# Kernel optimization log

Hardware: AMD Instinct MI355X
Metric: run time of the kernel (lower is better)

Reference implementation:

```python
import jax, jax.numpy as jnp
import numpy as np

N = 100000      # nodes
E = 1600000     # edges
F_IN = 128
HID = 64
N_CLS = 40


def setup_inputs() -> dict:
    key = jax.random.key(0)
    ks = jax.random.split(key, 8)
    x = jax.random.normal(ks[0], (N, F_IN), dtype=jnp.float32)
    edge_index = jax.random.randint(ks[1], (2, E), 0, N, dtype=jnp.int64)
    # SAGEConv params: lin_l (applied to mean-aggregated neighbors, with bias),
    # lin_r (applied to root/self features, no bias). Glorot-ish init scaling.
    W1_l = jax.random.normal(ks[2], (F_IN, HID), dtype=jnp.float32) / np.sqrt(F_IN)
    b1 = jnp.zeros((HID,), dtype=jnp.float32)
    W1_r = jax.random.normal(ks[3], (F_IN, HID), dtype=jnp.float32) / np.sqrt(F_IN)
    W2_l = jax.random.normal(ks[4], (HID, N_CLS), dtype=jnp.float32) / np.sqrt(HID)
    b2 = jnp.zeros((N_CLS,), dtype=jnp.float32)
    W2_r = jax.random.normal(ks[5], (HID, N_CLS), dtype=jnp.float32) / np.sqrt(HID)
    return {"x": x, "edge_index": edge_index,
            "W1_l": W1_l, "b1": b1, "W1_r": W1_r,
            "W2_l": W2_l, "b2": b2, "W2_r": W2_r}


def _sage_conv(x, src, dst, W_l, b_l, W_r):
    # mean aggregation of neighbor features: messages flow src -> dst
    msgs = x[src]                                              # [E, d]
    summed = jax.ops.segment_sum(msgs, dst, num_segments=N)    # [N, d]
    cnt = jax.ops.segment_sum(jnp.ones((src.shape[0],), x.dtype), dst,
                              num_segments=N)                  # [N]
    agg = summed / jnp.maximum(cnt, 1.0)[:, None]
    return agg @ W_l + b_l + x @ W_r


def reference(x, edge_index, W1_l, b1, W1_r, W2_l, b2, W2_r):
    src, dst = edge_index[0], edge_index[1]
    h = jax.nn.relu(_sage_conv(x, src, dst, W1_l, b1, W1_r))
    # dropout: identity in eval mode
    logits = _sage_conv(h, src, dst, W2_l, b2, W2_r)
    return jax.nn.log_softmax(logits, axis=1)
```

## Files before the change

### kernel.cpp

```cpp
#include <hip/hip_runtime.h>
#include <math.h>

#define N_NODES 100000
#define F_IN    128
#define HID     64
#define N_CLS   40
#define MT      (N_NODES / 16)

#define BSHIFT  9
#define BSZ     512
#define NB      ((N_NODES + BSZ - 1) / BSZ)
#define EPB     4096

typedef __attribute__((ext_vector_type(8))) short bf8_t;
typedef __attribute__((ext_vector_type(4))) float f4_t;
typedef __attribute__((ext_vector_type(2))) float f2v_t;

typedef unsigned short ushort_t;
typedef unsigned int uint_t;
typedef unsigned char uchar_t;

__device__ __forceinline__ ushort_t f2b(float f) {
    union { float f; uint_t u; } c; c.f = f;
    uint_t u = c.u + 0x7FFFu + ((c.u >> 16) & 1u);
    return (ushort_t)(u >> 16);
}
__device__ __forceinline__ float b2f(ushort_t h) {
    union { uint_t u; float f; } c; c.u = ((uint_t)h) << 16;
    return c.f;
}

#if defined(__has_builtin)
#if __has_builtin(__builtin_amdgcn_cvt_pk_f32_fp8) && __has_builtin(__builtin_amdgcn_cvt_pk_fp8_f32)
#define HAVE_FP8_HW 1
#endif
#endif

__device__ __forceinline__ uchar_t fp8_enc(float v) {
#ifdef HAVE_FP8_HW
    return (uchar_t)(__builtin_amdgcn_cvt_pk_fp8_f32(v, v, 0, false) & 0xff);
#else
    union { float f; uint_t u; } c; c.f = v;
    uint_t s = c.u >> 31;
    float av = fabsf(v);
    if (av > 448.f) av = 448.f;
    int e;
    float m = frexpf(av, &e);
    int ee = e + 6;
    uchar_t r;
    if (av == 0.f) r = 0;
    else if (ee <= 0) {
        int q = (int)(av * 512.f + 0.5f);
        if (q > 7) q = 7;
        r = (uchar_t)q;
    } else {
        int q = (int)(m * 16.f + 0.5f);
        if (q == 16) { q = 8; ee += 1; }
        if (ee > 15) { ee = 15; q = 15; }
        r = (uchar_t)((ee << 3) | (q & 7));
    }
    return r | (uchar_t)(s << 7);
#endif
}

__device__ __forceinline__ f2v_t fp8x2_dec_lo(uint_t w) {
#ifdef HAVE_FP8_HW
    return __builtin_amdgcn_cvt_pk_f32_fp8(w, false);
#else
    f2v_t r;
    for (int k = 0; k < 2; ++k) {
        uchar_t b = (w >> (8 * k)) & 0xff;
        uint_t s = (b >> 7) & 1, e = (b >> 3) & 15, m = b & 7;
        float f;
        if (e) { union { uint_t u; float ff; } c;
                 c.u = (s << 31) | ((e + 120) << 23) | (m << 20); f = c.ff; }
        else   { f = (float)m * 0.001953125f; if (s) f = -f; }
        r[k] = f;
    }
    return r;
#endif
}
__device__ __forceinline__ f2v_t fp8x2_dec_hi(uint_t w) {
#ifdef HAVE_FP8_HW
    return __builtin_amdgcn_cvt_pk_f32_fp8(w, true);
#else
    return fp8x2_dec_lo(w >> 16);
#endif
}

__global__ void block_hist_kernel(const int* __restrict__ ei, int E,
                                  int* __restrict__ blockHist) {
    __shared__ int cnt[NB];
    int t = threadIdx.x, blk = blockIdx.x;
    for (int i = t; i < NB; i += 256) cnt[i] = 0;
    __syncthreads();
    int e0 = blk * EPB;
#pragma unroll
    for (int i = 0; i < EPB / 256; ++i) {
        int e = e0 + i * 256 + t;
        if (e < E) atomicAdd(&cnt[ei[E + e] >> BSHIFT], 1);
    }
    __syncthreads();
    for (int i = t; i < NB; i += 256) blockHist[blk * NB + i] = cnt[i];
}

__global__ void col_scan_kernel(const int* __restrict__ blockHist, int nblk,
                                int* __restrict__ blockBase,
                                int* __restrict__ btot) {
    __shared__ int ss[256];
    __shared__ int carry;
    int bin = blockIdx.x, t = threadIdx.x;
    if (t == 0) carry = 0;
    __syncthreads();
    for (int c0 = 0; c0 < nblk; c0 += 256) {
        int b = c0 + t;
        int v = (b < nblk) ? blockHist[b * NB + bin] : 0;
        ss[t] = v;
        __syncthreads();
        for (int off = 1; off < 256; off <<= 1) {
            int u = (t >= off) ? ss[t - off] : 0;
            __syncthreads();
            ss[t] += u;
            __syncthreads();
        }
        if (b < nblk) blockBase[b * NB + bin] = carry + ss[t] - v;
        __syncthreads();
        if (t == 255) carry += ss[255];
        __syncthreads();
    }
    if (t == 0) btot[bin] = carry;
}

__global__ void scatter_pairs_kernel(const int* __restrict__ ei, int E,
                                     const int* __restrict__ blockBase,
                                     const int* __restrict__ btot,
                                     uint_t* __restrict__ pairs) {
    __shared__ int cur[NB];
    __shared__ int base[NB];
    __shared__ int ss[256];
    int t = threadIdx.x, blk = blockIdx.x;
    int v = (t < NB) ? btot[t] : 0;
    ss[t] = v;
    __syncthreads();
    for (int off = 1; off < 256; off <<= 1) {
        int u = (t >= off) ? ss[t - off] : 0;
        __syncthreads();
        ss[t] += u;
        __syncthreads();
    }
    if (t < NB) {
        cur[t] = 0;
        base[t] = (ss[t] - v) + blockBase[blk * NB + t];
    }
    __syncthreads();
    int e0 = blk * EPB;
#pragma unroll
    for (int i = 0; i < EPB / 256; ++i) {
        int e = e0 + i * 256 + t;
        if (e < E) {
            int src = ei[e];
            int dst = ei[E + e];
            int bin = dst >> BSHIFT;
            int r = atomicAdd(&cur[bin], 1);
            pairs[base[bin] + r] = ((uint_t)src << BSHIFT) | (uint_t)(dst & (BSZ - 1));
        }
    }
}

__global__ void bucket_sort_kernel(const uint_t* __restrict__ pairs,
                                   const int* __restrict__ btot,
                                   int* __restrict__ rowptr,
                                   int* __restrict__ csr) {
    __shared__ int hist[BSZ];
    __shared__ int lofs[BSZ];
    int bin = blockIdx.x, t = threadIdx.x;
    int pv = (t < NB) ? btot[t] : 0;
    lofs[t] = pv;
    __syncthreads();
    for (int off = 1; off < BSZ; off <<= 1) {
        int u = (t >= off) ? lofs[t - off] : 0;
        __syncthreads();
        lofs[t] += u;
        __syncthreads();
    }
    int base = (bin > 0) ? lofs[bin - 1] : 0;
    int cnt = btot[bin];
    __syncthreads();
    hist[t] = 0;
    __syncthreads();
    for (int i = t; i < cnt; i += BSZ)
        atomicAdd(&hist[pairs[base + i] & (BSZ - 1)], 1);
    __syncthreads();
    int v = hist[t];
    lofs[t] = v;
    __syncthreads();
    for (int off = 1; off < BSZ; off <<= 1) {
        int u = (t >= off) ? lofs[t - off] : 0;
        __syncthreads();
        lofs[t] += u;
        __syncthreads();
    }
    int excl = lofs[t] - v;
    int d_global = (bin << BSHIFT) + t;
    if (d_global < N_NODES) rowptr[d_global] = base + excl;
    if (bin == NB - 1 && t == 0) rowptr[N_NODES] = base + cnt;
    __syncthreads();
    lofs[t] = excl;
    hist[t] = 0;
    __syncthreads();
    for (int i = t; i < cnt; i += BSZ) {
        uint_t p = pairs[base + i];
        int lb = p & (BSZ - 1);
        int r = atomicAdd(&hist[lb], 1);
        csr[base + lofs[lb] + r] = (int)(p >> BSHIFT);
    }
}

__global__ void cvt_w_kernel(const float* __restrict__ W1l,
                             const float* __restrict__ W1r,
                             const float* __restrict__ W2l,
                             const float* __restrict__ W2r,
                             ushort_t* __restrict__ W1t,
                             ushort_t* __restrict__ W2t) {
    int t = blockIdx.x * blockDim.x + threadIdx.x;
    if (t < 128 * F_IN) {
        int n = t / F_IN, k = t - n * F_IN;
        float v = (n < HID) ? W1l[k * HID + n] : W1r[k * HID + (n - HID)];
        W1t[t] = f2b(v);
    } else if (t < 128 * F_IN + 80 * HID) {
        int u = t - 128 * F_IN;
        int n = u / HID, k = u - n * HID;
        float v = (n < N_CLS) ? W2l[k * N_CLS + n] : W2r[k * N_CLS + (n - N_CLS)];
        W2t[u] = f2b(v);
    }
}

__global__ void gemm1_mfma_kernel(const float* __restrict__ x,
                                  const ushort_t* __restrict__ W1t,
                                  uchar_t* __restrict__ y1f8,
                                  ushort_t* __restrict__ z1b) {
    __shared__ uchar_t sy[64][80];
    __shared__ ushort_t sz[64][72];
    int tid = threadIdx.x;
    int wave = tid >> 6, lane = tid & 63;
    int tile = blockIdx.x * 4 + wave;
    int m0b = blockIdx.x * 64;
    if (tile < MT) {
        int m0 = tile * 16;
        int r = lane & 15, q = lane >> 4;
        const float* xr = x + (size_t)(m0 + r) * F_IN + q * 8;
        bf8_t a[4];
#pragma unroll
        for (int kt = 0; kt < 4; ++kt) {
            float4 u = *(const float4*)(xr + kt * 32);
            float4 v = *(const float4*)(xr + kt * 32 + 4);
            bf8_t tt;
            tt[0] = (short)f2b(u.x); tt[1] = (short)f2b(u.y);
            tt[2] = (short)f2b(u.z); tt[3] = (short)f2b(u.w);
            tt[4] = (short)f2b(v.x); tt[5] = (short)f2b(v.y);
            tt[6] = (short)f2b(v.z); tt[7] = (short)f2b(v.w);
            a[kt] = tt;
        }
        int lr0 = wave * 16 + q * 4;
#pragma unroll
        for (int tn = 0; tn < 8; ++tn) {
            const ushort_t* wr = W1t + (size_t)(tn * 16 + r) * F_IN + q * 8;
            f4_t acc = {0.f, 0.f, 0.f, 0.f};
#pragma unroll
            for (int kt = 0; kt < 4; ++kt) {
                bf8_t b = *(const bf8_t*)(wr + kt * 32);
                acc = __builtin_amdgcn_mfma_f32_16x16x32_bf16(a[kt], b, acc, 0, 0, 0);
            }
            int col = tn * 16 + r;
            if (col < 64) {
#pragma unroll
                for (int rr = 0; rr < 4; ++rr)
                    sy[lr0 + rr][col] = fp8_enc(acc[rr]);
            } else {
#pragma unroll
                for (int rr = 0; rr < 4; ++rr)
                    sz[lr0 + rr][col - 64] = f2b(acc[rr]);
            }
        }
    }
    __syncthreads();
    int vrows = N_NODES - m0b; if (vrows > 64) vrows = 64;
    for (int idx = tid; idx < vrows * 4; idx += 256) {
        int row = idx >> 2, c = (idx & 3) << 4;
        *(uint4*)(y1f8 + (size_t)(m0b + row) * 64 + c) = *(const uint4*)&sy[row][c];
    }
    for (int idx = tid; idx < vrows * 8; idx += 256) {
        int row = idx >> 3, c = (idx & 7) << 3;
        *(uint4*)(z1b + (size_t)(m0b + row) * HID + c) = *(const uint4*)&sz[row][c];
    }
}

__device__ __forceinline__ void acc16(float* acc, uint4 v) {
    f2v_t p;
    p = fp8x2_dec_lo(v.x); acc[0]  += p[0]; acc[1]  += p[1];
    p = fp8x2_dec_hi(v.x); acc[2]  += p[0]; acc[3]  += p[1];
    p = fp8x2_dec_lo(v.y); acc[4]  += p[0]; acc[5]  += p[1];
    p = fp8x2_dec_hi(v.y); acc[6]  += p[0]; acc[7]  += p[1];
    p = fp8x2_dec_lo(v.z); acc[8]  += p[0]; acc[9]  += p[1];
    p = fp8x2_dec_hi(v.z); acc[10] += p[0]; acc[11] += p[1];
    p = fp8x2_dec_lo(v.w); acc[12] += p[0]; acc[13] += p[1];
    p = fp8x2_dec_hi(v.w); acc[14] += p[0]; acc[15] += p[1];
}

__global__ void agg1_kernel(const int* __restrict__ rowptr,
                            const int* __restrict__ csr,
                            const uchar_t* __restrict__ y1f8,
                            const ushort_t* __restrict__ z1b,
                            const float* __restrict__ b1,
                            ushort_t* __restrict__ hb) {
    int gid = blockIdx.x * blockDim.x + threadIdx.x;
    int wave = gid >> 6, lane = gid & 63;
    int g = lane >> 2, l = lane & 3;
    int n = wave * 16 + g;
    if (n >= N_NODES) return;
    int beg = rowptr[n], end = rowptr[n + 1];
    float acc[16];
#pragma unroll
    for (int j = 0; j < 16; ++j) acc[j] = 0.f;
    const uchar_t* yb = y1f8 + l * 16;
    int i = beg;
    for (; i + 3 < end; i += 4) {
        int s0 = csr[i], s1 = csr[i + 1], s2 = csr[i + 2], s3 = csr[i + 3];
        uint4 w0 = *(const uint4*)(yb + (size_t)s0 * 64);
        uint4 w1 = *(const uint4*)(yb + (size_t)s1 * 64);
        uint4 w2 = *(const uint4*)(yb + (size_t)s2 * 64);
        uint4 w3 = *(const uint4*)(yb + (size_t)s3 * 64);
        acc16(acc, w0); acc16(acc, w1); acc16(acc, w2); acc16(acc, w3);
    }
    for (; i < end; ++i) {
        uint4 w = *(const uint4*)(yb + (size_t)csr[i] * 64);
        acc16(acc, w);
    }
    float inv = 1.0f / fmaxf((float)(end - beg), 1.0f);
    int c = l * 16;
    ushort_t zz[16];
    *(uint4*)&zz[0] = *(const uint4*)(z1b + (size_t)n * HID + c);
    *(uint4*)&zz[8] = *(const uint4*)(z1b + (size_t)n * HID + c + 8);
    float bv[16];
    *(float4*)&bv[0]  = *(const float4*)(b1 + c);
    *(float4*)&bv[4]  = *(const float4*)(b1 + c + 4);
    *(float4*)&bv[8]  = *(const float4*)(b1 + c + 8);
    *(float4*)&bv[12] = *(const float4*)(b1 + c + 12);
    ushort_t o[16];
#pragma unroll
    for (int j = 0; j < 16; ++j) {
        float r = fmaxf(fmaf(acc[j], inv, bv[j] + b2f(zz[j])), 0.f);
        o[j] = f2b(r);
    }
    *(uint4*)(hb + (size_t)n * HID + c)     = *(const uint4*)&o[0];
    *(uint4*)(hb + (size_t)n * HID + c + 8) = *(const uint4*)&o[8];
}

__global__ void gemm2_mfma_kernel(const ushort_t* __restrict__ hb,
                                  const ushort_t* __restrict__ W2t,
                                  uchar_t* __restrict__ y2f8,
                                  ushort_t* __restrict__ z2b) {
    __shared__ uchar_t sy2[64 * 40];
    __shared__ ushort_t sz2[64][56];
    int tid = threadIdx.x;
    int wave = tid >> 6, lane = tid & 63;
    int tile = blockIdx.x * 4 + wave;
    int m0b = blockIdx.x * 64;
    if (tile < MT) {
        int m0 = tile * 16;
        int r = lane & 15, q = lane >> 4;
        const ushort_t* hr = hb + (size_t)(m0 + r) * HID + q * 8;
        bf8_t a[2];
#pragma unroll
        for (int kt = 0; kt < 2; ++kt)
            a[kt] = *(const bf8_t*)(hr + kt * 32);
        int lr0 = wave * 16 + q * 4;
#pragma unroll
        for (int tn = 0; tn < 5; ++tn) {
            const ushort_t* wr = W2t + (size_t)(tn * 16 + r) * HID + q * 8;
            f4_t acc = {0.f, 0.f, 0.f, 0.f};
#pragma unroll
            for (int kt = 0; kt < 2; ++kt) {
                bf8_t b = *(const bf8_t*)(wr + kt * 32);
                acc = __builtin_amdgcn_mfma_f32_16x16x32_bf16(a[kt], b, acc, 0, 0, 0);
            }
            int col = tn * 16 + r;
            if (col < N_CLS) {
#pragma unroll
                for (int rr = 0; rr < 4; ++rr)
                    sy2[(lr0 + rr) * 40 + col] = fp8_enc(acc[rr]);
            } else {
#pragma unroll
                for (int rr = 0; rr < 4; ++rr)
                    sz2[lr0 + rr][col - N_CLS] = f2b(acc[rr]);
            }
        }
    }
    __syncthreads();
    int vrows = N_NODES - m0b; if (vrows > 64) vrows = 64;
    int nch = (vrows * 40) >> 4;
    for (int idx = tid; idx < nch; idx += 256)
        *(uint4*)(y2f8 + (size_t)m0b * 40 + idx * 16) = *(const uint4*)&sy2[idx * 16];
    for (int idx = tid; idx < vrows * 5; idx += 256) {
        int row = idx / 5, c = (idx - row * 5) * 8;
        *(uint4*)(z2b + (size_t)(m0b + row) * HID + c) = *(const uint4*)&sz2[row][c];
    }
}

__global__ void agg2_kernel(const int* __restrict__ rowptr,
                            const int* __restrict__ csr,
                            const uchar_t* __restrict__ y2f8,
                            const ushort_t* __restrict__ z2b,
                            const float* __restrict__ b2,
                            float* __restrict__ out) {
    int gid = blockIdx.x * blockDim.x + threadIdx.x;
    int wave = gid >> 6, lane = gid & 63;
    int g = lane >> 4, l = lane & 15;
    int n = wave * 4 + g;
    if (n >= N_NODES) return;
    int beg = rowptr[n], end = rowptr[n + 1];
    float a0 = 0.f, a1 = 0.f, a2 = 0.f, a3 = 0.f;
    float4 bb = make_float4(0.f, 0.f, 0.f, 0.f);
    ushort4 zz; zz.x = 0; zz.y = 0; zz.z = 0; zz.w = 0;
    int c0 = l * 4;
    if (l < 10) {
        int i = beg;
        for (; i + 7 < end; i += 8) {
            int s0 = csr[i],     s1 = csr[i + 1], s2 = csr[i + 2], s3 = csr[i + 3];
            int s4 = csr[i + 4], s5 = csr[i + 5], s6 = csr[i + 6], s7 = csr[i + 7];
            uint_t w0 = *(const uint_t*)(y2f8 + (size_t)s0 * 40 + c0);
            uint_t w1 = *(const uint_t*)(y2f8 + (size_t)s1 * 40 + c0);
            uint_t w2 = *(const uint_t*)(y2f8 + (size_t)s2 * 40 + c0);
            uint_t w3 = *(const uint_t*)(y2f8 + (size_t)s3 * 40 + c0);
            uint_t w4 = *(const uint_t*)(y2f8 + (size_t)s4 * 40 + c0);
            uint_t w5 = *(const uint_t*)(y2f8 + (size_t)s5 * 40 + c0);
            uint_t w6 = *(const uint_t*)(y2f8 + (size_t)s6 * 40 + c0);
            uint_t w7 = *(const uint_t*)(y2f8 + (size_t)s7 * 40 + c0);
            f2v_t p;
            p = fp8x2_dec_lo(w0); a0 += p[0]; a1 += p[1];
            p = fp8x2_dec_hi(w0); a2 += p[0]; a3 += p[1];
            p = fp8x2_dec_lo(w1); a0 += p[0]; a1 += p[1];
            p = fp8x2_dec_hi(w1); a2 += p[0]; a3 += p[1];
            p = fp8x2_dec_lo(w2); a0 += p[0]; a1 += p[1];
            p = fp8x2_dec_hi(w2); a2 += p[0]; a3 += p[1];
            p = fp8x2_dec_lo(w3); a0 += p[0]; a1 += p[1];
            p = fp8x2_dec_hi(w3); a2 += p[0]; a3 += p[1];
            p = fp8x2_dec_lo(w4); a0 += p[0]; a1 += p[1];
            p = fp8x2_dec_hi(w4); a2 += p[0]; a3 += p[1];
            p = fp8x2_dec_lo(w5); a0 += p[0]; a1 += p[1];
            p = fp8x2_dec_hi(w5); a2 += p[0]; a3 += p[1];
            p = fp8x2_dec_lo(w6); a0 += p[0]; a1 += p[1];
            p = fp8x2_dec_hi(w6); a2 += p[0]; a3 += p[1];
            p = fp8x2_dec_lo(w7); a0 += p[0]; a1 += p[1];
            p = fp8x2_dec_hi(w7); a2 += p[0]; a3 += p[1];
        }
        for (; i + 3 < end; i += 4) {
            int s0 = csr[i], s1 = csr[i + 1], s2 = csr[i + 2], s3 = csr[i + 3];
            uint_t w0 = *(const uint_t*)(y2f8 + (size_t)s0 * 40 + c0);
            uint_t w1 = *(const uint_t*)(y2f8 + (size_t)s1 * 40 + c0);
            uint_t w2 = *(const uint_t*)(y2f8 + (size_t)s2 * 40 + c0);
            uint_t w3 = *(const uint_t*)(y2f8 + (size_t)s3 * 40 + c0);
            f2v_t p;
            p = fp8x2_dec_lo(w0); a0 += p[0]; a1 += p[1];
            p = fp8x2_dec_hi(w0); a2 += p[0]; a3 += p[1];
            p = fp8x2_dec_lo(w1); a0 += p[0]; a1 += p[1];
            p = fp8x2_dec_hi(w1); a2 += p[0]; a3 += p[1];
            p = fp8x2_dec_lo(w2); a0 += p[0]; a1 += p[1];
            p = fp8x2_dec_hi(w2); a2 += p[0]; a3 += p[1];
            p = fp8x2_dec_lo(w3); a0 += p[0]; a1 += p[1];
            p = fp8x2_dec_hi(w3); a2 += p[0]; a3 += p[1];
        }
        for (; i < end; ++i) {
            uint_t w = *(const uint_t*)(y2f8 + (size_t)csr[i] * 40 + c0);
            f2v_t p0 = fp8x2_dec_lo(w), p1 = fp8x2_dec_hi(w);
            a0 += p0[0]; a1 += p0[1]; a2 += p1[0]; a3 += p1[1];
        }
        bb = *(const float4*)(b2 + c0);
        zz = *(const ushort4*)(z2b + (size_t)n * HID + c0);
    }
    float inv = 1.0f / fmaxf((float)(end - beg), 1.0f);
    float v0 = (c0 + 0 < N_CLS) ? fmaf(a0, inv, bb.x + b2f(zz.x)) : -INFINITY;
    float v1 = (c0 + 1 < N_CLS) ? fmaf(a1, inv, bb.y + b2f(zz.y)) : -INFINITY;
    float v2 = (c0 + 2 < N_CLS) ? fmaf(a2, inv, bb.z + b2f(zz.z)) : -INFINITY;
    float v3 = (c0 + 3 < N_CLS) ? fmaf(a3, inv, bb.w + b2f(zz.w)) : -INFINITY;

    float m = fmaxf(fmaxf(v0, v1), fmaxf(v2, v3));
#pragma unroll
    for (int off = 1; off < 16; off <<= 1)
        m = fmaxf(m, __shfl_xor(m, off, 64));
    float s = 0.f;
    if (v0 > -INFINITY) s += expf(v0 - m);
    if (v1 > -INFINITY) s += expf(v1 - m);
    if (v2 > -INFINITY) s += expf(v2 - m);
    if (v3 > -INFINITY) s += expf(v3 - m);
#pragma unroll
    for (int off = 1; off < 16; off <<= 1)
        s += __shfl_xor(s, off, 64);
    float ls = logf(s);
    if (l < 10) {
        float4 o = make_float4(v0 - m - ls, v1 - m - ls, v2 - m - ls, v3 - m - ls);
        *(float4*)(out + (size_t)n * N_CLS + c0) = o;
    }
}

extern "C" void kernel_launch(void* const* d_in, const int* in_sizes, int n_in,
                              void* d_out, int out_size, void* d_ws, size_t ws_size,
                              hipStream_t stream) {
    const float* x   = (const float*)d_in[0];
    const int*   ei  = (const int*)d_in[1];
    const float* W1l = (const float*)d_in[2];
    const float* b1  = (const float*)d_in[3];
    const float* W1r = (const float*)d_in[4];
    const float* W2l = (const float*)d_in[5];
    const float* b2  = (const float*)d_in[6];
    const float* W2r = (const float*)d_in[7];
    float* out = (float*)d_out;
    const int E = in_sizes[1] / 2;
    const int nblk = (E + EPB - 1) / EPB;

    char* p = (char*)d_ws;
    auto take = [&](size_t bytes) {
        char* q = p;
        p += (bytes + 15) & ~(size_t)15;
        return (void*)q;
    };
    int* rowptr     = (int*)take(sizeof(int) * (N_NODES + 4));
    int* blockHist  = (int*)take(sizeof(int) * (size_t)nblk * NB);
    int* blockBase  = (int*)take(sizeof(int) * (size_t)nblk * NB);
    int* btot       = (int*)take(sizeof(int) * NB);
    uint_t* pairs   = (uint_t*)take(sizeof(uint_t) * (size_t)E);
    int* csr        = (int*)take(sizeof(int) * (size_t)E);
    ushort_t* W1t   = (ushort_t*)take(sizeof(ushort_t) * 128 * F_IN);
    ushort_t* W2t   = (ushort_t*)take(sizeof(ushort_t) * 80 * HID);
    uchar_t* y1f8   = (uchar_t*)take(sizeof(uchar_t) * (size_t)N_NODES * 64);
    ushort_t* z1b   = (ushort_t*)take(sizeof(ushort_t) * (size_t)N_NODES * HID);
    ushort_t* hb    = (ushort_t*)take(sizeof(ushort_t) * (size_t)N_NODES * HID);
    uchar_t* y2f8 = y1f8;
    ushort_t* z2b = z1b;

    const int B = 256;

    block_hist_kernel<<<nblk, 256, 0, stream>>>(ei, E, blockHist);
    col_scan_kernel<<<NB, 256, 0, stream>>>(blockHist, nblk, blockBase, btot);
    scatter_pairs_kernel<<<nblk, 256, 0, stream>>>(ei, E, blockBase, btot, pairs);
    bucket_sort_kernel<<<NB, BSZ, 0, stream>>>(pairs, btot, rowptr, csr);

    cvt_w_kernel<<<(128 * F_IN + 80 * HID + B - 1) / B, B, 0, stream>>>(
        W1l, W1r, W2l, W2r, W1t, W2t);

    int gemm_blocks = (MT + 3) / 4;
    int t_agg1 = (N_NODES / 16) * 64;
    int t_agg2 = (N_NODES / 4) * 64;

    gemm1_mfma_kernel<<<gemm_blocks, B, 0, stream>>>(x, W1t, y1f8, z1b);
    agg1_kernel<<<(t_agg1 + B - 1) / B, B, 0, stream>>>(rowptr, csr, y1f8, z1b, b1, hb);
    gemm2_mfma_kernel<<<gemm_blocks, B, 0, stream>>>(hb, W2t, y2f8, z2b);
    agg2_kernel<<<(t_agg2 + B - 1) / B, B, 0, stream>>>(rowptr, csr, y2f8, z2b, b2, out);
}
```

Measured before the change: 238.7 us.

## Replace two-level bucket sort CSR build with global-atomic degree count and scatter

Replaces the block-histogram, column-scan, pair-scatter and per-bucket sort pipeline with a simpler CSR construction. It counts in-degrees with global atomics, runs a three-stage prefix scan to get rowptr, then scatters source ids with per-node atomic cursors. This drops the intermediate pairs buffer and the serial column scans, at the cost of 1.6M contended global atomics twice and a nondeterministic neighbor order within each row.

```diff
diff --git a/kernel.cpp b/kernel.cpp
--- a/kernel.cpp
+++ b/kernel.cpp
@@ -6,11 +6,7 @@
 #define HID     64
 #define N_CLS   40
 #define MT      (N_NODES / 16)
-
-#define BSHIFT  9
-#define BSZ     512
-#define NB      ((N_NODES + BSZ - 1) / BSZ)
-#define EPB     4096
+#define NS1     ((N_NODES + 1023) / 1024)
 
 typedef __attribute__((ext_vector_type(8))) short bf8_t;
 typedef __attribute__((ext_vector_type(4))) float f4_t;
@@ -88,59 +84,29 @@
 #endif
 }
 
-__global__ void block_hist_kernel(const int* __restrict__ ei, int E,
-                                  int* __restrict__ blockHist) {
-    __shared__ int cnt[NB];
-    int t = threadIdx.x, blk = blockIdx.x;
-    for (int i = t; i < NB; i += 256) cnt[i] = 0;
-    __syncthreads();
-    int e0 = blk * EPB;
-#pragma unroll
-    for (int i = 0; i < EPB / 256; ++i) {
-        int e = e0 + i * 256 + t;
-        if (e < E) atomicAdd(&cnt[ei[E + e] >> BSHIFT], 1);
-    }
-    __syncthreads();
-    for (int i = t; i < NB; i += 256) blockHist[blk * NB + i] = cnt[i];
-}
-
-__global__ void col_scan_kernel(const int* __restrict__ blockHist, int nblk,
-                                int* __restrict__ blockBase,
-                                int* __restrict__ btot) {
+__global__ void zero_deg_kernel(int* __restrict__ deg) {
+    int i = (blockIdx.x * 256 + threadIdx.x) * 4;
+    if (i < N_NODES) *(int4*)(deg + i) = make_int4(0, 0, 0, 0);
+}
+
+__global__ void deg_count_kernel(const int* __restrict__ ei, int E,
+                                 int* __restrict__ deg) {
+    int e = blockIdx.x * blockDim.x + threadIdx.x;
+    int step = gridDim.x * blockDim.x;
+    for (; e < E; e += step)
+        atomicAdd(&deg[ei[E + e]], 1);
+}
+
+__global__ void scan1_kernel(const int* __restrict__ deg,
+                             int* __restrict__ rowptr,
+                             int* __restrict__ bsum) {
     __shared__ int ss[256];
-    __shared__ int carry;
-    int bin = blockIdx.x, t = threadIdx.x;
-    if (t == 0) carry = 0;
-    __syncthreads();
-    for (int c0 = 0; c0 < nblk; c0 += 256) {
-        int b = c0 + t;
-        int v = (b < nblk) ? blockHist[b * NB + bin] : 0;
-        ss[t] = v;
-        __syncthreads();
-        for (int off = 1; off < 256; off <<= 1) {
-            int u = (t >= off) ? ss[t - off] : 0;
-            __syncthreads();
-            ss[t] += u;
-            __syncthreads();
-        }
-        if (b < nblk) blockBase[b * NB + bin] = carry + ss[t] - v;
-        __syncthreads();
-        if (t == 255) carry += ss[255];
-        __syncthreads();
-    }
-    if (t == 0) btot[bin] = carry;
-}
-
-__global__ void scatter_pairs_kernel(const int* __restrict__ ei, int E,
-                                     const int* __restrict__ blockBase,
-                                     const int* __restrict__ btot,
-                                     uint_t* __restrict__ pairs) {
-    __shared__ int cur[NB];
-    __shared__ int base[NB];
-    __shared__ int ss[256];
-    int t = threadIdx.x, blk = blockIdx.x;
-    int v = (t < NB) ? btot[t] : 0;
-    ss[t] = v;
+    int b = blockIdx.x, t = threadIdx.x;
+    int i0 = b * 1024 + t * 4;
+    int4 d = make_int4(0, 0, 0, 0);
+    if (i0 < N_NODES) d = *(const int4*)(deg + i0);
+    int s = d.x + d.y + d.z + d.w;
+    ss[t] = s;
     __syncthreads();
     for (int off = 1; off < 256; off <<= 1) {
         int u = (t >= off) ? ss[t - off] : 0;
@@ -148,71 +114,57 @@
         ss[t] += u;
         __syncthreads();
     }
-    if (t < NB) {
-        cur[t] = 0;
-        base[t] = (ss[t] - v) + blockBase[blk * NB + t];
-    }
+    int excl = ss[t] - s;
+    if (t == 255) bsum[b] = ss[255];
+    if (i0 < N_NODES) {
+        int4 o;
+        o.x = excl; o.y = excl + d.x; o.z = o.y + d.y; o.w = o.z + d.z;
+        *(int4*)(rowptr + i0) = o;
+    }
+}
+
+__global__ void scan2_kernel(const int* __restrict__ bsum,
+                             int* __restrict__ bbase,
+                             int* __restrict__ rowptr) {
+    __shared__ int ss[128];
+    int t = threadIdx.x;
+    int v = (t < NS1) ? bsum[t] : 0;
+    ss[t] = v;
     __syncthreads();
-    int e0 = blk * EPB;
-#pragma unroll
-    for (int i = 0; i < EPB / 256; ++i) {
-        int e = e0 + i * 256 + t;
-        if (e < E) {
-            int src = ei[e];
-            int dst = ei[E + e];
-            int bin = dst >> BSHIFT;
-            int r = atomicAdd(&cur[bin], 1);
-            pairs[base[bin] + r] = ((uint_t)src << BSHIFT) | (uint_t)(dst & (BSZ - 1));
-        }
-    }
-}
-
-__global__ void bucket_sort_kernel(const uint_t* __restrict__ pairs,
-                                   const int* __restrict__ btot,
-                                   int* __restrict__ rowptr,
+    for (int off = 1; off < 128; off <<= 1) {
+        int u = (t >= off) ? ss[t - off] : 0;
+        __syncthreads();
+        ss[t] += u;
+        __syncthreads();
+    }
+    if (t < NS1) bbase[t] = ss[t] - v;
+    if (t == 127) rowptr[N_NODES] = ss[127];
+}
+
+__global__ void scan3_kernel(int* __restrict__ rowptr,
+                             const int* __restrict__ bbase,
+                             int* __restrict__ cur) {
+    int b = blockIdx.x, t = threadIdx.x;
+    int i0 = b * 1024 + t * 4;
+    if (i0 < N_NODES) {
+        int base = bbase[b];
+        int4 r = *(const int4*)(rowptr + i0);
+        r.x += base; r.y += base; r.z += base; r.w += base;
+        *(int4*)(rowptr + i0) = r;
+        *(int4*)(cur + i0) = r;
+    }
+}
+
+__global__ void scatter_csr_kernel(const int* __restrict__ ei, int E,
+                                   int* __restrict__ cur,
                                    int* __restrict__ csr) {
-    __shared__ int hist[BSZ];
-    __shared__ int lofs[BSZ];
-    int bin = blockIdx.x, t = threadIdx.x;
-    int pv = (t < NB) ? btot[t] : 0;
-    lofs[t] = pv;
-    __syncthreads();
-    for (int off = 1; off < BSZ; off <<= 1) {
-        int u = (t >= off) ? lofs[t - off] : 0;
-        __syncthreads();
-        lofs[t] += u;
-        __syncthreads();
-    }
-    int base = (bin > 0) ? lofs[bin - 1] : 0;
-    int cnt = btot[bin];
-    __syncthreads();
-    hist[t] = 0;
-    __syncthreads();
-    for (int i = t; i < cnt; i += BSZ)
-        atomicAdd(&hist[pairs[base + i] & (BSZ - 1)], 1);
-    __syncthreads();
-    int v = hist[t];
-    lofs[t] = v;
-    __syncthreads();
-    for (int off = 1; off < BSZ; off <<= 1) {
-        int u = (t >= off) ? lofs[t - off] : 0;
-        __syncthreads();
-        lofs[t] += u;
-        __syncthreads();
-    }
-    int excl = lofs[t] - v;
-    int d_global = (bin << BSHIFT) + t;
-    if (d_global < N_NODES) rowptr[d_global] = base + excl;
-    if (bin == NB - 1 && t == 0) rowptr[N_NODES] = base + cnt;
-    __syncthreads();
-    lofs[t] = excl;
-    hist[t] = 0;
-    __syncthreads();
-    for (int i = t; i < cnt; i += BSZ) {
-        uint_t p = pairs[base + i];
-        int lb = p & (BSZ - 1);
-        int r = atomicAdd(&hist[lb], 1);
-        csr[base + lofs[lb] + r] = (int)(p >> BSHIFT);
+    int e = blockIdx.x * blockDim.x + threadIdx.x;
+    int step = gridDim.x * blockDim.x;
+    for (; e < E; e += step) {
+        int s = ei[e];
+        int d = ei[E + e];
+        int pos = atomicAdd(&cur[d], 1);
+        csr[pos] = s;
     }
 }
 
@@ -516,7 +468,6 @@
     const float* W2r = (const float*)d_in[7];
     float* out = (float*)d_out;
     const int E = in_sizes[1] / 2;
-    const int nblk = (E + EPB - 1) / EPB;
 
     char* p = (char*)d_ws;
     auto take = [&](size_t bytes) {
@@ -525,10 +476,10 @@
         return (void*)q;
     };
     int* rowptr     = (int*)take(sizeof(int) * (N_NODES + 4));
-    int* blockHist  = (int*)take(sizeof(int) * (size_t)nblk * NB);
-    int* blockBase  = (int*)take(sizeof(int) * (size_t)nblk * NB);
-    int* btot       = (int*)take(sizeof(int) * NB);
-    uint_t* pairs   = (uint_t*)take(sizeof(uint_t) * (size_t)E);
+    int* deg        = (int*)take(sizeof(int) * N_NODES);
+    int* cur        = (int*)take(sizeof(int) * N_NODES);
+    int* bsum       = (int*)take(sizeof(int) * 128);
+    int* bbase      = (int*)take(sizeof(int) * 128);
     int* csr        = (int*)take(sizeof(int) * (size_t)E);
     ushort_t* W1t   = (ushort_t*)take(sizeof(ushort_t) * 128 * F_IN);
     ushort_t* W2t   = (ushort_t*)take(sizeof(ushort_t) * 80 * HID);
@@ -540,10 +491,12 @@
 
     const int B = 256;
 
-    block_hist_kernel<<<nblk, 256, 0, stream>>>(ei, E, blockHist);
-    col_scan_kernel<<<NB, 256, 0, stream>>>(blockHist, nblk, blockBase, btot);
-    scatter_pairs_kernel<<<nblk, 256, 0, stream>>>(ei, E, blockBase, btot, pairs);
-    bucket_sort_kernel<<<NB, BSZ, 0, stream>>>(pairs, btot, rowptr, csr);
+    zero_deg_kernel<<<NS1, B, 0, stream>>>(deg);
+    deg_count_kernel<<<1024, B, 0, stream>>>(ei, E, deg);
+    scan1_kernel<<<NS1, B, 0, stream>>>(deg, rowptr, bsum);
+    scan2_kernel<<<1, 128, 0, stream>>>(bsum, bbase, rowptr);
+    scan3_kernel<<<NS1, B, 0, stream>>>(rowptr, bbase, cur);
+    scatter_csr_kernel<<<1024, B, 0, stream>>>(ei, E, cur, csr);
 
     cvt_w_kernel<<<(128 * F_IN + 80 * HID + B - 1) / B, B, 0, stream>>>(
         W1l, W1r, W2l, W2r, W1t, W2t);
```

New measurement: 400.9 us. 67.9% more time.
